# Optimization experiments

Hardware: AMD Instinct MI355X
Metric: run time of the kernel (lower is better)

Reference implementation:

```python
import jax, jax.numpy as jnp
import numpy as np

B, S, HID = 4, 1024, 2048
H, KV, D = 16, 4, 128  # query heads, kv heads, head_dim
ROPE_THETA = 1e6


def setup_inputs() -> dict:
    key = jax.random.key(0)
    ks = jax.random.split(key, 5)
    x = jax.random.normal(ks[0], (B, S, HID), dtype=jnp.float32)
    wq = jax.random.normal(ks[1], (HID, H * D), dtype=jnp.float32) / np.sqrt(HID)
    wk = jax.random.normal(ks[2], (HID, KV * D), dtype=jnp.float32) / np.sqrt(HID)
    wv = jax.random.normal(ks[3], (HID, KV * D), dtype=jnp.float32) / np.sqrt(HID)
    wo = jax.random.normal(ks[4], (H * D, HID), dtype=jnp.float32) / np.sqrt(H * D)
    # RoPE tables: freqs duplicated to head_dim (HF convention matching rotate_half)
    inv_freq = 1.0 / (ROPE_THETA ** (jnp.arange(0, D, 2, dtype=jnp.float32) / D))
    ang = jnp.arange(S, dtype=jnp.float32)[:, None] * inv_freq[None, :]  # [S, D/2]
    emb = jnp.concatenate([ang, ang], axis=-1)  # [S, D]
    return {"x": x, "cos": jnp.cos(emb), "sin": jnp.sin(emb),
            "wq": wq, "wk": wk, "wv": wv, "wo": wo}


def _rotate_half(t):
    half = t.shape[-1] // 2
    return jnp.concatenate([-t[..., half:], t[..., :half]], axis=-1)


def reference(x, cos, sin, wq, wk, wv, wo):
    b, s, _ = x.shape
    q = (x @ wq).reshape(b, s, H, D)
    k = (x @ wk).reshape(b, s, KV, D)
    v = (x @ wv).reshape(b, s, KV, D)
    # RoPE: cos/sin [S,D] broadcast over heads (unsqueeze_dim=1 -> [S,1,D])
    c = cos[:, None, :]
    sn = sin[:, None, :]
    q = q * c + _rotate_half(q) * sn
    k = k * c + _rotate_half(k) * sn
    # repeat_kv: each kv head repeated n_repeat times consecutively
    rep = H // KV
    k = jnp.repeat(k, rep, axis=2)  # [B,S,H,D]
    v = jnp.repeat(v, rep, axis=2)
    # [B,H,S,D]
    q = q.transpose(0, 2, 1, 3)
    k = k.transpose(0, 2, 1, 3)
    v = v.transpose(0, 2, 1, 3)
    scores = jnp.einsum("bhqd,bhkd->bhqk", q, k) / jnp.sqrt(jnp.float32(D))
    causal = jnp.tril(jnp.ones((s, s), dtype=bool))
    scores = jnp.where(causal, scores, -jnp.inf)
    probs = jax.nn.softmax(scores.astype(jnp.float32), axis=-1).astype(q.dtype)
    out = jnp.einsum("bhqk,bhkd->bhqd", probs, v)
    out = out.transpose(0, 2, 1, 3).reshape(b, s, H * D)
    return out @ wo
```

## Files before the change

kernel.cpp:

```cpp
#include <hip/hip_runtime.h>

typedef __attribute__((ext_vector_type(8))) __bf16 bf16x8;
typedef __attribute__((ext_vector_type(4))) __bf16 bf16x4;
typedef __attribute__((ext_vector_type(4))) float f32x4;

#define DEV static __device__ __forceinline__

DEV void gload_lds16(const void* g, void* l) {
  __builtin_amdgcn_global_load_lds((const __attribute__((address_space(1))) void*)g,
                                   (__attribute__((address_space(3))) void*)l, 16, 0, 0);
}

DEV void lgkm0_sb() {
  asm volatile("s_waitcnt lgkmcnt(0)" ::: "memory");
  __builtin_amdgcn_sched_barrier(0);
}

__global__ void cvt_kernel(const float* __restrict__ src, __bf16* __restrict__ dst, int n) {
  int i = (blockIdx.x * 256 + threadIdx.x) * 8;
  if (i >= n) return;
  float4 a = *(const float4*)(src + i);
  float4 b = *(const float4*)(src + i + 4);
  bf16x8 o;
  o[0] = (__bf16)a.x; o[1] = (__bf16)a.y; o[2] = (__bf16)a.z; o[3] = (__bf16)a.w;
  o[4] = (__bf16)b.x; o[5] = (__bf16)b.y; o[6] = (__bf16)b.z; o[7] = (__bf16)b.w;
  *(bf16x8*)(dst + i) = o;
}

__global__ void tcvt_kernel(const float* __restrict__ src, __bf16* __restrict__ dst, int K, int N) {
  __shared__ float tile[32][33];
  int k0 = blockIdx.y * 32, n0 = blockIdx.x * 32;
  int tx = threadIdx.x & 31, ty = threadIdx.x >> 5;
  #pragma unroll
  for (int i = 0; i < 32; i += 8)
    tile[ty + i][tx] = src[(size_t)(k0 + ty + i) * N + n0 + tx];
  __syncthreads();
  #pragma unroll
  for (int i = 0; i < 32; i += 8)
    dst[(size_t)(n0 + ty + i) * K + k0 + tx] = (__bf16)tile[tx][ty + i];
}

__global__ void vt_kernel(const __bf16* __restrict__ QKV, __bf16* __restrict__ VT) {
  __shared__ __bf16 t[32][33];
  int sx = blockIdx.x;
  int dx = blockIdx.y;
  int bk = blockIdx.z;
  int b = bk >> 2, kvh = bk & 3;
  int tx = threadIdx.x & 31, ty = threadIdx.x >> 5;
  #pragma unroll
  for (int i = 0; i < 32; i += 8)
    t[ty + i][tx] = QKV[(size_t)(b * 1024 + sx * 32 + ty + i) * 3072 + 2560 + kvh * 128 + dx * 32 + tx];
  __syncthreads();
  #pragma unroll
  for (int i = 0; i < 32; i += 8)
    VT[((size_t)bk * 128 + dx * 32 + ty + i) * 1024 + sx * 32 + tx] = t[tx][ty + i];
}

__global__ __launch_bounds__(512, 2) void gemm8p_qkv(const __bf16* __restrict__ A,
                                                     const __bf16* __restrict__ Bt,
                                                     __bf16* __restrict__ C,
                                                     int M, int N, int K) {
  constexpr int ABYTES = 256 * 64 * 2;
  constexpr int BBYTES = 192 * 64 * 2;
  __shared__ alignas(1024) char smem[2 * (ABYTES + BBYTES)];

  const int tid = threadIdx.x;
  const int l = tid & 63, w = tid >> 6;
  const int wr = w >> 2, wc = w & 3;
  const int g = l >> 4, ln = l & 15;

  const int nbx = gridDim.x;
  const int nwg = nbx * gridDim.y;
  int lin = blockIdx.y * nbx + blockIdx.x;
  lin = (lin & 7) * (nwg >> 3) + (lin >> 3);
  const int brow = (lin / nbx) * 256, bcol = (lin % nbx) * 192;

  const __bf16* Ag = A + (size_t)brow * K;
  const __bf16* Bg = Bt + (size_t)bcol * K;
  const int NT = K / 64;

  auto Abuf = [&](int buf) -> char* { return smem + buf * ABYTES; };
  auto Bbuf = [&](int buf) -> char* { return smem + 2 * ABYTES + buf * BBYTES; };

  f32x4 acc[8][3] = {};

  auto chunk = [&](const __bf16* gb, char* lb, int ktc, int sub) {
    int r16 = l >> 2;
    int colb = ((l & 3) * 16) ^ (((l >> 5) & 1) << 5);
    int row = (sub >> 1) * 16 + r16;
    gload_lds16(gb + (size_t)row * K + ktc * 64 + (sub & 1) * 32 + (colb >> 1),
                lb + sub * 1024 + l * 16);
  };
  auto stA0 = [&](int ktc, int buf) {
    #pragma unroll
    for (int i = 0; i < 2; ++i) { int idx = i * 8 + w; chunk(Ag, Abuf(buf), ktc, (idx >> 3) * 16 + (idx & 7)); }
  };
  auto stA1 = [&](int ktc, int buf) {
    #pragma unroll
    for (int i = 0; i < 2; ++i) { int idx = i * 8 + w; chunk(Ag, Abuf(buf), ktc, 8 + (idx >> 3) * 16 + (idx & 7)); }
  };
  auto stBg0 = [&](int ktc, int buf) {
    #pragma unroll
    for (int i = 0; i < 2; ++i) {
      int t = i * 8 + w;
      int sub = ((t >> 2) * 3 + ((t >> 1) & 1)) * 2 + (t & 1);
      chunk(Bg, Bbuf(buf), ktc, sub);
    }
  };
  auto stBg1 = [&](int ktc, int buf) {
    int sub = ((w >> 1) * 3 + 2) * 2 + (w & 1);
    chunk(Bg, Bbuf(buf), ktc, sub);
  };

  auto ldA = [&](int buf, int m, int kk) -> bf16x8 {
    int sub = (wr * 8 + m) * 2 + kk;
    return *(const bf16x8*)(Abuf(buf) + sub * 1024 + ln * 64 + ((g * 16) ^ (((ln >> 3) & 1) << 5)));
  };
  auto ldB = [&](int buf, int nf, int kk) -> bf16x8 {
    int sub = (wc * 3 + nf) * 2 + kk;
    return *(const bf16x8*)(Bbuf(buf) + sub * 1024 + ln * 64 + ((g * 16) ^ (((ln >> 3) & 1) << 5)));
  };

  auto bar = [&]() {
    __builtin_amdgcn_sched_barrier(0);
    __builtin_amdgcn_s_barrier();
    __builtin_amdgcn_sched_barrier(0);
  };

  stA0(0, 0); stBg0(0, 0); stBg1(0, 0); stA1(0, 0);
  stA0(1, 1); stBg0(1, 1); stBg1(1, 1); stA1(1, 1);
  asm volatile("s_waitcnt vmcnt(10)" ::: "memory");
  __builtin_amdgcn_sched_barrier(0);
  bar();

  bf16x8 af[4][2], bfv[3][2];

  for (int kt = 0; kt < NT; ++kt) {
    const int buf = kt & 1;
    const int ktc = (kt + 2) & 31;

    #pragma unroll
    for (int m = 0; m < 4; ++m) { af[m][0] = ldA(buf, m, 0); af[m][1] = ldA(buf, m, 1); }
    #pragma unroll
    for (int nf = 0; nf < 2; ++nf) { bfv[nf][0] = ldB(buf, nf, 0); bfv[nf][1] = ldB(buf, nf, 1); }
    bar();
    lgkm0_sb();
    __builtin_amdgcn_s_setprio(1);
    #pragma unroll
    for (int m = 0; m < 4; ++m)
      #pragma unroll
      for (int nf = 0; nf < 2; ++nf)
        #pragma unroll
        for (int kk = 0; kk < 2; ++kk)
          acc[m][nf] = __builtin_amdgcn_mfma_f32_16x16x32_bf16(af[m][kk], bfv[nf][kk], acc[m][nf], 0, 0, 0);
    __builtin_amdgcn_s_setprio(0);
    asm volatile("s_waitcnt vmcnt(9)" ::: "memory");
    __builtin_amdgcn_sched_barrier(0);
    bar();

    bfv[2][0] = ldB(buf, 2, 0); bfv[2][1] = ldB(buf, 2, 1);
    stA0(ktc, buf); stBg0(ktc, buf);
    bar();
    lgkm0_sb();
    __builtin_amdgcn_s_setprio(1);
    #pragma unroll
    for (int m = 0; m < 4; ++m)
      #pragma unroll
      for (int kk = 0; kk < 2; ++kk)
        acc[m][2] = __builtin_amdgcn_mfma_f32_16x16x32_bf16(af[m][kk], bfv[2][kk], acc[m][2], 0, 0, 0);
    __builtin_amdgcn_s_setprio(0);
    asm volatile("s_waitcnt vmcnt(11)" ::: "memory");
    __builtin_amdgcn_sched_barrier(0);
    bar();

    #pragma unroll
    for (int m = 0; m < 4; ++m) { af[m][0] = ldA(buf, 4 + m, 0); af[m][1] = ldA(buf, 4 + m, 1); }
    stBg1(ktc, buf);
    bar();
    lgkm0_sb();
    __builtin_amdgcn_s_setprio(1);
    #pragma unroll
    for (int m = 0; m < 4; ++m)
      #pragma unroll
      for (int nf = 0; nf < 2; ++nf)
        #pragma unroll
        for (int kk = 0; kk < 2; ++kk)
          acc[4 + m][nf] = __builtin_amdgcn_mfma_f32_16x16x32_bf16(af[m][kk], bfv[nf][kk], acc[4 + m][nf], 0, 0, 0);
    __builtin_amdgcn_s_setprio(0);
    bar();

    stA1(ktc, buf);
    bar();
    lgkm0_sb();
    __builtin_amdgcn_s_setprio(1);
    #pragma unroll
    for (int m = 0; m < 4; ++m)
      #pragma unroll
      for (int kk = 0; kk < 2; ++kk)
        acc[4 + m][2] = __builtin_amdgcn_mfma_f32_16x16x32_bf16(af[m][kk], bfv[2][kk], acc[4 + m][2], 0, 0, 0);
    __builtin_amdgcn_s_setprio(0);
    asm volatile("s_waitcnt vmcnt(10)" ::: "memory");
    __builtin_amdgcn_sched_barrier(0);
    bar();
  }

  #pragma unroll
  for (int mi = 0; mi < 8; ++mi)
    #pragma unroll
    for (int nf = 0; nf < 3; ++nf)
      #pragma unroll
      for (int j = 0; j < 4; ++j) {
        size_t r = brow + wr * 128 + mi * 16 + g * 4 + j;
        size_t c = bcol + wc * 48 + nf * 16 + ln;
        C[r * N + c] = (__bf16)acc[mi][nf][j];
      }
}

__global__ __launch_bounds__(512, 2) void gemm2p(const __bf16* __restrict__ A,
                                                 const __bf16* __restrict__ Bt,
                                                 float* __restrict__ C,
                                                 int M, int N, int K) {
  constexpr int ABYTES = 256 * 64 * 2;
  constexpr int BBYTES = 128 * 64 * 2;
  __shared__ alignas(1024) char smem[2 * (ABYTES + BBYTES)];

  const int tid = threadIdx.x;
  const int l = tid & 63, w = tid >> 6;
  const int wr = w >> 1, wc = w & 1;
  const int g = l >> 4, ln = l & 15;

  const int nbx = gridDim.x;
  const int nwg = nbx * gridDim.y;
  int lin = blockIdx.y * nbx + blockIdx.x;
  lin = (lin & 7) * (nwg >> 3) + (lin >> 3);
  const int brow = (lin / nbx) * 256, bcol = (lin % nbx) * 128;

  const __bf16* Ag = A + (size_t)brow * K;
  const __bf16* Bg = Bt + (size_t)bcol * K;
  const int NT = K / 64;

  auto Abuf = [&](int buf) -> char* { return smem + buf * ABYTES; };
  auto Bbuf = [&](int buf) -> char* { return smem + 2 * ABYTES + buf * BBYTES; };

  f32x4 acc[4][4] = {};

  auto chunk = [&](const __bf16* gb, char* lb, int ktc, int sub) {
    int r16 = l >> 2;
    int colb = ((l & 3) * 16) ^ (((l >> 5) & 1) << 5);
    int row = (sub >> 1) * 16 + r16;
    gload_lds16(gb + (size_t)row * K + ktc * 64 + (sub & 1) * 32 + (colb >> 1),
                lb + sub * 1024 + l * 16);
  };
  auto stAp0 = [&](int ktc, int buf) {
    #pragma unroll
    for (int i = 0; i < 2; ++i) { int t = i * 8 + w; chunk(Ag, Abuf(buf), ktc, (t >> 2) * 8 + (t & 3)); }
  };
  auto stAp1 = [&](int ktc, int buf) {
    #pragma unroll
    for (int i = 0; i < 2; ++i) { int t = i * 8 + w; chunk(Ag, Abuf(buf), ktc, (t >> 2) * 8 + 4 + (t & 3)); }
  };
  auto stB = [&](int ktc, int buf) {
    #pragma unroll
    for (int i = 0; i < 2; ++i) { int t = i * 8 + w; chunk(Bg, Bbuf(buf), ktc, t); }
  };

  auto ldA = [&](int buf, int mi, int kk) -> bf16x8 {
    int sub = (wr * 4 + mi) * 2 + kk;
    return *(const bf16x8*)(Abuf(buf) + sub * 1024 + ln * 64 + ((g * 16) ^ (((ln >> 3) & 1) << 5)));
  };
  auto ldB = [&](int buf, int nf, int kk) -> bf16x8 {
    int sub = (wc * 4 + nf) * 2 + kk;
    return *(const bf16x8*)(Bbuf(buf) + sub * 1024 + ln * 64 + ((g * 16) ^ (((ln >> 3) & 1) << 5)));
  };

  auto vm6 = [&]() {
    asm volatile("s_waitcnt vmcnt(6)" ::: "memory");
    __builtin_amdgcn_sched_barrier(0);
  };
  auto bar = [&]() {
    __builtin_amdgcn_sched_barrier(0);
    __builtin_amdgcn_s_barrier();
    __builtin_amdgcn_sched_barrier(0);
  };

  stAp0(0, 0); stB(0, 0);
  stAp1(0, 0);
  stAp0(1, 1); stB(1, 1);
  vm6();
  bar();

  bf16x8 af[2][2], bfv[4][2];

  for (int kt = 0; kt < NT; ++kt) {
    const int buf = kt & 1;
    const int ktc1 = (kt + 1) & 31;
    const int ktc2 = (kt + 2) & 31;

    #pragma unroll
    for (int mi = 0; mi < 2; ++mi) { af[mi][0] = ldA(buf, mi, 0); af[mi][1] = ldA(buf, mi, 1); }
    #pragma unroll
    for (int nf = 0; nf < 4; ++nf) { bfv[nf][0] = ldB(buf, nf, 0); bfv[nf][1] = ldB(buf, nf, 1); }
    stAp1(ktc1, buf ^ 1);
    bar();
    lgkm0_sb();
    __builtin_amdgcn_s_setprio(1);
    #pragma unroll
    for (int mi = 0; mi < 2; ++mi)
      #pragma unroll
      for (int nf = 0; nf < 4; ++nf)
        #pragma unroll
        for (int kk = 0; kk < 2; ++kk)
          acc[mi][nf] = __builtin_amdgcn_mfma_f32_16x16x32_bf16(af[mi][kk], bfv[nf][kk], acc[mi][nf], 0, 0, 0);
    __builtin_amdgcn_s_setprio(0);
    vm6();
    bar();

    #pragma unroll
    for (int mi = 0; mi < 2; ++mi) { af[mi][0] = ldA(buf, 2 + mi, 0); af[mi][1] = ldA(buf, 2 + mi, 1); }
    stAp0(ktc2, buf); stB(ktc2, buf);
    bar();
    lgkm0_sb();
    __builtin_amdgcn_s_setprio(1);
    #pragma unroll
    for (int mi = 0; mi < 2; ++mi)
      #pragma unroll
      for (int nf = 0; nf < 4; ++nf)
        #pragma unroll
        for (int kk = 0; kk < 2; ++kk)
          acc[2 + mi][nf] = __builtin_amdgcn_mfma_f32_16x16x32_bf16(af[mi][kk], bfv[nf][kk], acc[2 + mi][nf], 0, 0, 0);
    __builtin_amdgcn_s_setprio(0);
    vm6();
    bar();
  }

  #pragma unroll
  for (int mi = 0; mi < 4; ++mi)
    #pragma unroll
    for (int nf = 0; nf < 4; ++nf)
      #pragma unroll
      for (int j = 0; j < 4; ++j) {
        size_t r = brow + wr * 64 + mi * 16 + g * 4 + j;
        size_t c = bcol + wc * 64 + nf * 16 + ln;
        C[r * N + c] = acc[mi][nf][j];
      }
}

__global__ void ropek_kernel(__bf16* __restrict__ QKV, const float* __restrict__ cosb,
                             const float* __restrict__ sinb) {
  int gid = blockIdx.x * 256 + threadIdx.x;
  int p = gid & 15;
  int ht = gid >> 4;
  int hc = ht & 3;
  int tok = ht >> 2;
  int s = tok & 1023;
  __bf16* base = QKV + (size_t)tok * 3072 + 2048 + hc * 128;
  int d0 = p * 4;
  const float* cr = cosb + s * 128;
  const float* sr = sinb + s * 128;
  float x0[4], x1[4];
  #pragma unroll
  for (int j = 0; j < 4; ++j) {
    x0[j] = (float)base[d0 + j];
    x1[j] = (float)base[d0 + 64 + j];
  }
  #pragma unroll
  for (int j = 0; j < 4; ++j) {
    float n0 = x0[j] * cr[d0 + j] - x1[j] * sr[d0 + j];
    float n1 = x1[j] * cr[d0 + 64 + j] + x0[j] * sr[d0 + 64 + j];
    base[d0 + j] = (__bf16)n0;
    base[d0 + 64 + j] = (__bf16)n1;
  }
}

__global__ __launch_bounds__(256, 2) void attn_kernel(const __bf16* __restrict__ QKV,
                                                      const __bf16* __restrict__ VT,
                                                      const float* __restrict__ cosb,
                                                      const float* __restrict__ sinb,
                                                      __bf16* __restrict__ AO) {
  __shared__ __bf16 Kl[2][64 * 128];
  __shared__ __bf16 Vt[128 * 64];
  __shared__ __bf16 Pl[4][16 * 72];

  const int tid = threadIdx.x, l = tid & 63, w = tid >> 6;
  const int h = blockIdx.y, b = blockIdx.z;
  const int kvh = h >> 2;
  const int g = l >> 4, ln = l & 15;
  const __bf16* VTg = VT + (size_t)(b * 4 + kvh) * 128 * 1024;
  const float scsc = 0.08838834764831845f;

  auto stageK = [&](int buf, int kt) {
    const __bf16* Kg = QKV + (size_t)(b * 1024 + kt * 64) * 3072 + 2048 + kvh * 128;
    #pragma unroll
    for (int i = 0; i < 4; ++i) {
      int r = i * 16 + (tid >> 4);
      int c = tid & 15;
      int csw = c ^ (r & 7);
      gload_lds16(Kg + (size_t)r * 3072 + csw * 8, (char*)&Kl[buf][0] + i * 4096 + tid * 16);
    }
  };
  auto stageV = [&](int kt) {
    #pragma unroll
    for (int i = 0; i < 4; ++i) {
      int ci = i * 256 + tid;
      int row = ci >> 3;
      int c = ci & 7;
      int csw = c ^ (row & 7);
      gload_lds16(VTg + (size_t)row * 1024 + kt * 64 + csw * 8, (char*)Vt + (size_t)ci * 16);
    }
  };

  #pragma unroll 1
  for (int pass = 0; pass < 2; ++pass) {
    const int qt = pass ? 15 - (int)blockIdx.x : (int)blockIdx.x;
    const size_t tokQ = (size_t)b * 1024 + qt * 64;
    const int srow = qt * 64 + w * 16 + ln;

    bf16x8 qf[4];
    {
      const __bf16* qp = QKV + (tokQ + w * 16 + ln) * 3072 + h * 128;
      bf16x8 qraw[4];
      #pragma unroll
      for (int ks = 0; ks < 4; ++ks) qraw[ks] = *(const bf16x8*)(qp + ks * 32 + g * 8);
      const float* cr = cosb + (size_t)srow * 128;
      const float* sr = sinb + (size_t)srow * 128;
      #pragma unroll
      for (int ks2 = 0; ks2 < 2; ++ks2)
        #pragma unroll
        for (int j = 0; j < 8; ++j) {
          int d = ks2 * 32 + g * 8 + j;
          float lo = (float)qraw[ks2][j], hi = (float)qraw[ks2 + 2][j];
          float c0 = cr[d], s0 = sr[d];
          qf[ks2][j]     = (__bf16)(lo * c0 - hi * s0);
          qf[ks2 + 2][j] = (__bf16)(hi * c0 + lo * s0);
        }
    }

    float mrow = -1e30f, lrow = 0.f;
    f32x4 acco[8] = {};

    stageK(0, 0);
    int cur = 0;

    for (int kt = 0; kt <= qt; ++kt) {
      __syncthreads();

      stageV(kt);
      if (kt < qt) stageK(cur ^ 1, kt + 1);

      f32x4 accs[4] = {};
      __builtin_amdgcn_s_setprio(1);
      #pragma unroll
      for (int cb = 0; cb < 4; ++cb) {
        int row = cb * 16 + ln;
        #pragma unroll
        for (int ks = 0; ks < 4; ++ks) {
          bf16x8 kb = *(const bf16x8*)((const char*)&Kl[cur][0] + row * 256 +
                                       (((ks * 4 + g) ^ (row & 7)) * 16));
          accs[cb] = __builtin_amdgcn_mfma_f32_16x16x32_bf16(kb, qf[ks], accs[cb], 0, 0, 0);
        }
      }
      __builtin_amdgcn_s_setprio(0);

      const bool diag = (kt == qt);
      #pragma unroll
      for (int cb = 0; cb < 4; ++cb)
        #pragma unroll
        for (int j = 0; j < 4; ++j) {
          float s = accs[cb][j] * scsc;
          if (diag && (cb * 16 + g * 4 + j > w * 16 + ln)) s = -1e30f;
          accs[cb][j] = s;
        }

      float mt = accs[0][0];
      #pragma unroll
      for (int cb = 0; cb < 4; ++cb)
        #pragma unroll
        for (int j = 0; j < 4; ++j) mt = fmaxf(mt, accs[cb][j]);
      mt = fmaxf(mt, __shfl_xor(mt, 16, 64));
      mt = fmaxf(mt, __shfl_xor(mt, 32, 64));
      float mnew = fmaxf(mrow, mt);
      float corr = __expf(mrow - mnew);
      mrow = mnew;
      float rs = 0.f;
      #pragma unroll
      for (int cb = 0; cb < 4; ++cb)
        #pragma unroll
        for (int j = 0; j < 4; ++j) {
          float p = __expf(accs[cb][j] - mnew);
          accs[cb][j] = p;
          rs += p;
        }
      rs += __shfl_xor(rs, 16, 64);
      rs += __shfl_xor(rs, 32, 64);
      lrow = lrow * corr + rs;
      #pragma unroll
      for (int n = 0; n < 8; ++n)
        #pragma unroll
        for (int j = 0; j < 4; ++j) acco[n][j] *= corr;

      #pragma unroll
      for (int cb = 0; cb < 4; ++cb) {
        bf16x4 pw;
        #pragma unroll
        for (int j = 0; j < 4; ++j) pw[j] = (__bf16)accs[cb][j];
        *(bf16x4*)(&Pl[w][ln * 72 + cb * 16 + g * 4]) = pw;
      }

      __syncthreads();

      __builtin_amdgcn_s_setprio(1);
      #pragma unroll
      for (int sc = 0; sc < 2; ++sc) {
        bf16x8 pa = *(const bf16x8*)(&Pl[w][ln * 72 + sc * 32 + g * 8]);
        #pragma unroll
        for (int n = 0; n < 8; ++n) {
          int row = n * 16 + ln;
          bf16x8 vb = *(const bf16x8*)((const char*)Vt + row * 128 +
                                       (((sc * 4 + g) ^ (row & 7)) * 16));
          acco[n] = __builtin_amdgcn_mfma_f32_16x16x32_bf16(vb, pa, acco[n], 0, 0, 0);
        }
      }
      __builtin_amdgcn_s_setprio(0);
      cur ^= 1;
    }

    float rl = 1.f / lrow;
    size_t r = tokQ + w * 16 + ln;
    #pragma unroll
    for (int n = 0; n < 8; ++n) {
      bf16x4 ov;
      #pragma unroll
      for (int j = 0; j < 4; ++j) ov[j] = (__bf16)(acco[n][j] * rl);
      *(bf16x4*)(&AO[r * 2048 + h * 128 + n * 16 + g * 4]) = ov;
    }
  }
}

extern "C" void kernel_launch(void* const* d_in, const int* in_sizes, int n_in,
                              void* d_out, int out_size, void* d_ws, size_t ws_size,
                              hipStream_t stream) {
  const float* x    = (const float*)d_in[0];
  const float* cosb = (const float*)d_in[1];
  const float* sinb = (const float*)d_in[2];
  const float* wq   = (const float*)d_in[3];
  const float* wk   = (const float*)d_in[4];
  const float* wv   = (const float*)d_in[5];
  const float* wo   = (const float*)d_in[6];
  float* out = (float*)d_out;

  char* ws = (char*)d_ws;
  const size_t OFF_XB    = 0;
  const size_t OFF_WQKVT = OFF_XB + 16777216;
  const size_t OFF_WOT   = OFF_WQKVT + 12582912;
  const size_t OFF_QKV   = OFF_WOT + 8388608;
  const size_t OFF_AO    = OFF_QKV + 25165824;
  const size_t OFF_VT    = OFF_XB;

  __bf16* Xb    = (__bf16*)(ws + OFF_XB);
  __bf16* WqkvT = (__bf16*)(ws + OFF_WQKVT);
  __bf16* WoT   = (__bf16*)(ws + OFF_WOT);
  __bf16* QKVb  = (__bf16*)(ws + OFF_QKV);
  __bf16* AOb   = (__bf16*)(ws + OFF_AO);
  __bf16* VTb   = (__bf16*)(ws + OFF_VT);

  cvt_kernel<<<4096 * 2048 / 8 / 256, 256, 0, stream>>>(x, Xb, 4096 * 2048);
  tcvt_kernel<<<dim3(64, 64), 256, 0, stream>>>(wq, WqkvT, 2048, 2048);
  tcvt_kernel<<<dim3(16, 64), 256, 0, stream>>>(wk, WqkvT + (size_t)2048 * 2048, 2048, 512);
  tcvt_kernel<<<dim3(16, 64), 256, 0, stream>>>(wv, WqkvT + (size_t)2560 * 2048, 2048, 512);
  tcvt_kernel<<<dim3(64, 64), 256, 0, stream>>>(wo, WoT, 2048, 2048);
  gemm8p_qkv<<<dim3(16, 16), 512, 0, stream>>>(Xb, WqkvT, QKVb, 4096, 3072, 2048);
  vt_kernel<<<dim3(32, 4, 16), 256, 0, stream>>>(QKVb, VTb);
  ropek_kernel<<<4096 * 4 * 16 / 256, 256, 0, stream>>>(QKVb, cosb, sinb);
  attn_kernel<<<dim3(8, 16, 4), 256, 0, stream>>>(QKVb, VTb, cosb, sinb, AOb);
  gemm2p<<<dim3(16, 16), 512, 0, stream>>>(AOb, WoT, out, 4096, 2048, 2048);
}
```

Baseline: 171.5 us.

## Rewrite QKV GEMM with square 256x256 tiles and 4-phase split-K pipeline

Replaces the 256x192 QKV projection GEMM with a templated 256x256-tile kernel that splits each 64-wide K tile into two 32-wide halves. Loads and MFMAs are interleaved in four phases, with prefetch of the next tiles issued between them. The grid shrinks from 256 to 192 workgroups. Larger tiles raise arithmetic intensity and data reuse per LDS load, at the cost of more accumulator registers, more LDS, and fewer workgroups, which may leave CUs underused on a 256-CU part.

```diff
diff --git a/kernel.cpp b/kernel.cpp
--- a/kernel.cpp
+++ b/kernel.cpp
@@ -56,13 +56,13 @@
     VT[((size_t)bk * 128 + dx * 32 + ty + i) * 1024 + sx * 32 + tx] = t[tx][ty + i];
 }
 
-__global__ __launch_bounds__(512, 2) void gemm8p_qkv(const __bf16* __restrict__ A,
-                                                     const __bf16* __restrict__ Bt,
-                                                     __bf16* __restrict__ C,
-                                                     int M, int N, int K) {
-  constexpr int ABYTES = 256 * 64 * 2;
-  constexpr int BBYTES = 192 * 64 * 2;
-  __shared__ alignas(1024) char smem[2 * (ABYTES + BBYTES)];
+template <typename OutT>
+__global__ __launch_bounds__(512, 2) void gemm4p(const __bf16* __restrict__ A,
+                                                 const __bf16* __restrict__ Bt,
+                                                 OutT* __restrict__ C,
+                                                 int M, int N, int K) {
+  constexpr int TBYTES = 256 * 64 * 2;
+  __shared__ alignas(1024) char smem[4 * TBYTES];
 
   const int tid = threadIdx.x;
   const int l = tid & 63, w = tid >> 6;
@@ -73,16 +73,16 @@
   const int nwg = nbx * gridDim.y;
   int lin = blockIdx.y * nbx + blockIdx.x;
   lin = (lin & 7) * (nwg >> 3) + (lin >> 3);
-  const int brow = (lin / nbx) * 256, bcol = (lin % nbx) * 192;
+  const int brow = (lin / nbx) * 256, bcol = (lin % nbx) * 256;
 
   const __bf16* Ag = A + (size_t)brow * K;
   const __bf16* Bg = Bt + (size_t)bcol * K;
   const int NT = K / 64;
 
-  auto Abuf = [&](int buf) -> char* { return smem + buf * ABYTES; };
-  auto Bbuf = [&](int buf) -> char* { return smem + 2 * ABYTES + buf * BBYTES; };
-
-  f32x4 acc[8][3] = {};
+  auto Abuf = [&](int buf) -> char* { return smem + buf * TBYTES; };
+  auto Bbuf = [&](int buf) -> char* { return smem + 2 * TBYTES + buf * TBYTES; };
+
+  f32x4 acc[8][4] = {};
 
   auto chunk = [&](const __bf16* gb, char* lb, int ktc, int sub) {
     int r16 = l >> 2;
@@ -91,128 +91,117 @@
     gload_lds16(gb + (size_t)row * K + ktc * 64 + (sub & 1) * 32 + (colb >> 1),
                 lb + sub * 1024 + l * 16);
   };
-  auto stA0 = [&](int ktc, int buf) {
-    #pragma unroll
-    for (int i = 0; i < 2; ++i) { int idx = i * 8 + w; chunk(Ag, Abuf(buf), ktc, (idx >> 3) * 16 + (idx & 7)); }
-  };
-  auto stA1 = [&](int ktc, int buf) {
-    #pragma unroll
-    for (int i = 0; i < 2; ++i) { int idx = i * 8 + w; chunk(Ag, Abuf(buf), ktc, 8 + (idx >> 3) * 16 + (idx & 7)); }
-  };
-  auto stBg0 = [&](int ktc, int buf) {
-    #pragma unroll
-    for (int i = 0; i < 2; ++i) {
-      int t = i * 8 + w;
-      int sub = ((t >> 2) * 3 + ((t >> 1) & 1)) * 2 + (t & 1);
-      chunk(Bg, Bbuf(buf), ktc, sub);
-    }
-  };
-  auto stBg1 = [&](int ktc, int buf) {
-    int sub = ((w >> 1) * 3 + 2) * 2 + (w & 1);
-    chunk(Bg, Bbuf(buf), ktc, sub);
-  };
-
-  auto ldA = [&](int buf, int m, int kk) -> bf16x8 {
-    int sub = (wr * 8 + m) * 2 + kk;
+  auto stA = [&](int ktc, int buf, int kk) {
+    #pragma unroll
+    for (int i = 0; i < 2; ++i) { int t = i * 8 + w; chunk(Ag, Abuf(buf), ktc, t * 2 + kk); }
+  };
+  auto stB = [&](int ktc, int buf, int kk) {
+    #pragma unroll
+    for (int i = 0; i < 2; ++i) { int t = i * 8 + w; chunk(Bg, Bbuf(buf), ktc, t * 2 + kk); }
+  };
+
+  auto ldA = [&](int buf, int mi, int kk) -> bf16x8 {
+    int sub = (wr * 8 + mi) * 2 + kk;
     return *(const bf16x8*)(Abuf(buf) + sub * 1024 + ln * 64 + ((g * 16) ^ (((ln >> 3) & 1) << 5)));
   };
   auto ldB = [&](int buf, int nf, int kk) -> bf16x8 {
-    int sub = (wc * 3 + nf) * 2 + kk;
+    int sub = (wc * 4 + nf) * 2 + kk;
     return *(const bf16x8*)(Bbuf(buf) + sub * 1024 + ln * 64 + ((g * 16) ^ (((ln >> 3) & 1) << 5)));
   };
 
+  auto vm6 = [&]() {
+    asm volatile("s_waitcnt vmcnt(6)" ::: "memory");
+    __builtin_amdgcn_sched_barrier(0);
+  };
   auto bar = [&]() {
     __builtin_amdgcn_sched_barrier(0);
     __builtin_amdgcn_s_barrier();
     __builtin_amdgcn_sched_barrier(0);
   };
 
-  stA0(0, 0); stBg0(0, 0); stBg1(0, 0); stA1(0, 0);
-  stA0(1, 1); stBg0(1, 1); stBg1(1, 1); stA1(1, 1);
-  asm volatile("s_waitcnt vmcnt(10)" ::: "memory");
-  __builtin_amdgcn_sched_barrier(0);
+  stA(0, 0, 0); stB(0, 0, 0); stB(0, 0, 1); stA(0, 0, 1);
+  stA(1, 1, 0); stB(1, 1, 0); stB(1, 1, 1);
+  vm6();
   bar();
 
-  bf16x8 af[4][2], bfv[3][2];
+  bf16x8 af[4], bfv[4];
 
   for (int kt = 0; kt < NT; ++kt) {
     const int buf = kt & 1;
-    const int ktc = (kt + 2) & 31;
-
-    #pragma unroll
-    for (int m = 0; m < 4; ++m) { af[m][0] = ldA(buf, m, 0); af[m][1] = ldA(buf, m, 1); }
-    #pragma unroll
-    for (int nf = 0; nf < 2; ++nf) { bfv[nf][0] = ldB(buf, nf, 0); bfv[nf][1] = ldB(buf, nf, 1); }
+    const int kt1 = (kt + 1) & 31;
+    const int kt2 = (kt + 2) & 31;
+
+    #pragma unroll
+    for (int mi = 0; mi < 4; ++mi) af[mi] = ldA(buf, mi, 0);
+    #pragma unroll
+    for (int nf = 0; nf < 4; ++nf) bfv[nf] = ldB(buf, nf, 0);
+    stA(kt1, buf ^ 1, 1);
     bar();
     lgkm0_sb();
     __builtin_amdgcn_s_setprio(1);
     #pragma unroll
-    for (int m = 0; m < 4; ++m)
-      #pragma unroll
-      for (int nf = 0; nf < 2; ++nf)
-        #pragma unroll
-        for (int kk = 0; kk < 2; ++kk)
-          acc[m][nf] = __builtin_amdgcn_mfma_f32_16x16x32_bf16(af[m][kk], bfv[nf][kk], acc[m][nf], 0, 0, 0);
+    for (int mi = 0; mi < 4; ++mi)
+      #pragma unroll
+      for (int nf = 0; nf < 4; ++nf)
+        acc[mi][nf] = __builtin_amdgcn_mfma_f32_16x16x32_bf16(af[mi], bfv[nf], acc[mi][nf], 0, 0, 0);
     __builtin_amdgcn_s_setprio(0);
-    asm volatile("s_waitcnt vmcnt(9)" ::: "memory");
-    __builtin_amdgcn_sched_barrier(0);
-    bar();
-
-    bfv[2][0] = ldB(buf, 2, 0); bfv[2][1] = ldB(buf, 2, 1);
-    stA0(ktc, buf); stBg0(ktc, buf);
+    bar();
+
+    #pragma unroll
+    for (int mi = 0; mi < 4; ++mi) af[mi] = ldA(buf, 4 + mi, 0);
+    stB(kt2, buf, 0);
     bar();
     lgkm0_sb();
     __builtin_amdgcn_s_setprio(1);
     #pragma unroll
-    for (int m = 0; m < 4; ++m)
-      #pragma unroll
-      for (int kk = 0; kk < 2; ++kk)
-        acc[m][2] = __builtin_amdgcn_mfma_f32_16x16x32_bf16(af[m][kk], bfv[2][kk], acc[m][2], 0, 0, 0);
+    for (int mi = 0; mi < 4; ++mi)
+      #pragma unroll
+      for (int nf = 0; nf < 4; ++nf)
+        acc[4 + mi][nf] = __builtin_amdgcn_mfma_f32_16x16x32_bf16(af[mi], bfv[nf], acc[4 + mi][nf], 0, 0, 0);
     __builtin_amdgcn_s_setprio(0);
-    asm volatile("s_waitcnt vmcnt(11)" ::: "memory");
-    __builtin_amdgcn_sched_barrier(0);
-    bar();
-
-    #pragma unroll
-    for (int m = 0; m < 4; ++m) { af[m][0] = ldA(buf, 4 + m, 0); af[m][1] = ldA(buf, 4 + m, 1); }
-    stBg1(ktc, buf);
+    bar();
+
+    #pragma unroll
+    for (int mi = 0; mi < 4; ++mi) af[mi] = ldA(buf, mi, 1);
+    #pragma unroll
+    for (int nf = 0; nf < 4; ++nf) bfv[nf] = ldB(buf, nf, 1);
+    stA(kt2, buf, 0);
     bar();
     lgkm0_sb();
     __builtin_amdgcn_s_setprio(1);
     #pragma unroll
-    for (int m = 0; m < 4; ++m)
-      #pragma unroll
-      for (int nf = 0; nf < 2; ++nf)
-        #pragma unroll
-        for (int kk = 0; kk < 2; ++kk)
-          acc[4 + m][nf] = __builtin_amdgcn_mfma_f32_16x16x32_bf16(af[m][kk], bfv[nf][kk], acc[4 + m][nf], 0, 0, 0);
+    for (int mi = 0; mi < 4; ++mi)
+      #pragma unroll
+      for (int nf = 0; nf < 4; ++nf)
+        acc[mi][nf] = __builtin_amdgcn_mfma_f32_16x16x32_bf16(af[mi], bfv[nf], acc[mi][nf], 0, 0, 0);
     __builtin_amdgcn_s_setprio(0);
     bar();
 
-    stA1(ktc, buf);
+    #pragma unroll
+    for (int mi = 0; mi < 4; ++mi) af[mi] = ldA(buf, 4 + mi, 1);
+    stB(kt2, buf, 1);
     bar();
     lgkm0_sb();
     __builtin_amdgcn_s_setprio(1);
     #pragma unroll
-    for (int m = 0; m < 4; ++m)
-      #pragma unroll
-      for (int kk = 0; kk < 2; ++kk)
-        acc[4 + m][2] = __builtin_amdgcn_mfma_f32_16x16x32_bf16(af[m][kk], bfv[2][kk], acc[4 + m][2], 0, 0, 0);
+    for (int mi = 0; mi < 4; ++mi)
+      #pragma unroll
+      for (int nf = 0; nf < 4; ++nf)
+        acc[4 + mi][nf] = __builtin_amdgcn_mfma_f32_16x16x32_bf16(af[mi], bfv[nf], acc[4 + mi][nf], 0, 0, 0);
     __builtin_amdgcn_s_setprio(0);
-    asm volatile("s_waitcnt vmcnt(10)" ::: "memory");
-    __builtin_amdgcn_sched_barrier(0);
+    vm6();
     bar();
   }
 
   #pragma unroll
   for (int mi = 0; mi < 8; ++mi)
     #pragma unroll
-    for (int nf = 0; nf < 3; ++nf)
+    for (int nf = 0; nf < 4; ++nf)
       #pragma unroll
       for (int j = 0; j < 4; ++j) {
         size_t r = brow + wr * 128 + mi * 16 + g * 4 + j;
-        size_t c = bcol + wc * 48 + nf * 16 + ln;
-        C[r * N + c] = (__bf16)acc[mi][nf][j];
+        size_t c = bcol + wc * 64 + nf * 16 + ln;
+        C[r * N + c] = (OutT)acc[mi][nf][j];
       }
 }
 
@@ -568,7 +557,7 @@
   tcvt_kernel<<<dim3(16, 64), 256, 0, stream>>>(wk, WqkvT + (size_t)2048 * 2048, 2048, 512);
   tcvt_kernel<<<dim3(16, 64), 256, 0, stream>>>(wv, WqkvT + (size_t)2560 * 2048, 2048, 512);
   tcvt_kernel<<<dim3(64, 64), 256, 0, stream>>>(wo, WoT, 2048, 2048);
-  gemm8p_qkv<<<dim3(16, 16), 512, 0, stream>>>(Xb, WqkvT, QKVb, 4096, 3072, 2048);
+  gemm4p<__bf16><<<dim3(12, 16), 512, 0, stream>>>(Xb, WqkvT, QKVb, 4096, 3072, 2048);
   vt_kernel<<<dim3(32, 4, 16), 256, 0, stream>>>(QKVb, VTb);
   ropek_kernel<<<4096 * 4 * 16 / 256, 256, 0, stream>>>(QKVb, cosb, sinb);
   attn_kernel<<<dim3(8, 16, 4), 256, 0, stream>>>(QKVb, VTb, cosb, sinb, AOb);
```

Measured after the change: 174.9 us. 1.02x slower.
